# Performance work log

Measured on AMD Instinct MI355X. Metric: run time of the kernel, lower is better.

Reference implementation:

```python
import jax, jax.numpy as jnp
import numpy as np

B, N, M, K = 4, 8192, 2048, 8
F1, F2 = 256, 256


def _knn_idx(p1t, p2t, k):
    # p1t [B,N,3], p2t [B,M,3] -> idx [B,N,k] of k nearest points in p2t for each p1t point
    d = (jnp.sum(p1t ** 2, -1)[:, :, None]
         + jnp.sum(p2t ** 2, -1)[:, None, :]
         - 2.0 * jnp.einsum('bnc,bmc->bnm', p1t, p2t))
    _, idx = jax.lax.top_k(-d, k)
    return idx


def _gather(feat, idx):
    # feat [B,C,M], idx [B,N,K] -> [B,C,N,K]  (grouping_operation)
    return jax.vmap(lambda f, i: f[:, i])(feat, idx)


def setup_inputs() -> dict:
    key = jax.random.key(0)
    ks = jax.random.split(key, 16)
    rn = lambda k, s: jax.random.normal(k, s, dtype=jnp.float32)
    ru = lambda k, s: jax.random.uniform(k, s, dtype=jnp.float32)
    return {
        'pos1': rn(ks[0], (B, 3, N)),
        'pos2': rn(ks[1], (B, 3, M)),
        'feature1': rn(ks[2], (B, F1, N)),
        'feature2': rn(ks[3], (B, F2, M)),
        'w1_0': rn(ks[4], (128, F2 + 3)) * 0.05, 's1_0': ru(ks[5], (128,)), 'b1_0': rn(ks[6], (128,)) * 0.05,
        'w1_1': rn(ks[7], (128, 128)) * 0.05, 's1_1': ru(ks[8], (128,)), 'b1_1': rn(ks[9], (128,)) * 0.05,
        'w1_2': rn(ks[10], (256, 128)) * 0.05, 's1_2': ru(ks[11], (256,)), 'b1_2': rn(ks[12], (256,)) * 0.05,
        'w2_0': rn(ks[13], (256, 256 + F1)) * 0.05, 's2_0': ru(ks[14], (256,)), 'b2_0': rn(ks[15], (256,)) * 0.05,
    }


def reference(pos1, pos2, feature1, feature2,
              w1_0, s1_0, b1_0, w1_1, s1_1, b1_1, w1_2, s1_2, b1_2,
              w2_0, s2_0, b2_0):
    # KNN grouping (knn=True branch): neighbors of each pos1 point among pos2 points
    idx = _knn_idx(pos1.transpose(0, 2, 1), pos2.transpose(0, 2, 1), K)  # [B,N,K]
    pos2_grouped = _gather(pos2, idx)                 # [B,3,N,K]
    pos_diff = pos2_grouped - pos1[:, :, :, None]     # [B,3,N,K]
    feat2_grouped = _gather(feature2, idx)            # [B,F2,N,K]
    feat = jnp.concatenate([feat2_grouped, pos_diff], axis=1)  # [B,F2+3,N,K]
    # mlp1: 1x1 Conv2d (no bias) + BN(eval, folded scale/bias) + ReLU
    for w, s, b in ((w1_0, s1_0, b1_0), (w1_1, s1_1, b1_1), (w1_2, s1_2, b1_2)):
        feat = jax.nn.relu(jnp.einsum('oc,bcnk->bonk', w, feat)
                           * s[None, :, None, None] + b[None, :, None, None])
    feat = jnp.max(feat, axis=-1)                     # [B,256,N]
    feat = jnp.concatenate([feat, feature1], axis=1)  # [B,256+F1,N]
    # mlp2: 1x1 Conv1d (no bias) + BN + ReLU
    for w, s, b in ((w2_0, s2_0, b2_0),):
        feat = jax.nn.relu(jnp.einsum('oc,bcn->bon', w, feat)
                           * s[None, :, None] + b[None, :, None])
    return feat
```

## Files before the change

### kernel.cpp

```cpp
#include <hip/hip_runtime.h>
#include <hip/hip_bf16.h>

#define B_ 4
#define N_ 8192
#define M_ 2048
#define K_ 8

typedef __bf16 bf16x8 __attribute__((ext_vector_type(8)));
typedef __bf16 bf16x4 __attribute__((ext_vector_type(4)));
typedef float  floatx4 __attribute__((ext_vector_type(4)));

__global__ __launch_bounds__(256) void prep_weights(
    const float* __restrict__ w10, const float* __restrict__ w11,
    const float* __restrict__ w12, const float* __restrict__ w20,
    __bf16* __restrict__ w0p, __bf16* __restrict__ w11b,
    __bf16* __restrict__ w12b, __bf16* __restrict__ w20b)
{
  int t = blockIdx.x * 256 + threadIdx.x;
  if (t < 36864) {
    int o = t / 288, c = t - o * 288;
    w0p[t] = (c < 259) ? (__bf16)w10[o * 259 + c] : (__bf16)0.0f;
  } else if (t < 53248) {
    int i = t - 36864; w11b[i] = (__bf16)w11[i];
  } else if (t < 86016) {
    int i = t - 53248; w12b[i] = (__bf16)w12[i];
  } else if (t < 217088) {
    int i = t - 86016; w20b[i] = (__bf16)w20[i];
  }
}

__global__ __launch_bounds__(256) void transpose_cast(
    const float* __restrict__ in, __bf16* __restrict__ out, int C, int L)
{
  __shared__ float tile[32][33];
  const int b = blockIdx.z;
  const int c0 = blockIdx.y * 32, l0 = blockIdx.x * 32;
  const int tx = threadIdx.x & 31, ty = threadIdx.x >> 5;
  const float* src = in + (size_t)b * C * L;
  #pragma unroll
  for (int i = 0; i < 4; i++)
    tile[ty + 8 * i][tx] = src[(size_t)(c0 + ty + 8 * i) * L + l0 + tx];
  __syncthreads();
  __bf16* dst = out + (size_t)b * L * C;
  #pragma unroll
  for (int i = 0; i < 4; i++)
    dst[(size_t)(l0 + ty + 8 * i) * C + c0 + tx] = (__bf16)tile[tx][ty + 8 * i];
}

__global__ __launch_bounds__(256) void knn_kernel(
    const float* __restrict__ pos1, const float* __restrict__ pos2,
    int* __restrict__ idx_out)
{
  __shared__ floatx4 P[M_];
  __shared__ float md[64][33];
  __shared__ int   mi[64][33];
  const int b = blockIdx.y;
  const int n0 = blockIdx.x * 64;
  const int tid = threadIdx.x;

  const float* p2 = pos2 + b * 3 * M_;
  for (int i = tid; i < M_; i += 256) {
    float x = p2[i], y = p2[M_ + i], z = p2[2 * M_ + i];
    floatx4 q;
    q[0] = x; q[1] = y; q[2] = z;
    q[3] = __fadd_rn(__fadd_rn(__fmul_rn(x, x), __fmul_rn(y, y)), __fmul_rn(z, z));
    P[i] = q;
  }
  __syncthreads();

  const int p = tid >> 2, t = tid & 3;
  const int n = n0 + p;
  const float* p1 = pos1 + b * 3 * N_;
  const float x1 = p1[n], y1 = p1[N_ + n], z1 = p1[2 * N_ + n];
  const float r1 = __fadd_rn(__fadd_rn(__fmul_rn(x1, x1), __fmul_rn(y1, y1)),
                             __fmul_rn(z1, z1));

  float bd[K_]; int bi[K_];
  #pragma unroll
  for (int j = 0; j < K_; j++) { bd[j] = 3.0e38f; bi[j] = 0; }

  for (int j = 0; j < 512; j += 4) {
    float d4[4]; int c4[4];
    #pragma unroll
    for (int jj = 0; jj < 4; jj++) {
      const int c = t + 4 * (j + jj);
      floatx4 q = P[c];
      float dot = __fadd_rn(__fadd_rn(__fmul_rn(x1, q[0]), __fmul_rn(y1, q[1])),
                            __fmul_rn(z1, q[2]));
      d4[jj] = __fsub_rn(__fadd_rn(r1, q[3]), __fmul_rn(2.0f, dot));
      c4[jj] = c;
    }
    #pragma unroll
    for (int jj = 0; jj < 4; jj++) {
      float d = d4[jj];
      if (d < bd[K_ - 1]) {
        float cd = d; int ci = c4[jj];
        #pragma unroll
        for (int q = 0; q < K_; q++) {
          bool lt = (cd < bd[q]);
          float nd = lt ? cd : bd[q];  int ni = lt ? ci : bi[q];
          float od = lt ? bd[q] : cd;  int oi = lt ? bi[q] : ci;
          bd[q] = nd; bi[q] = ni; cd = od; ci = oi;
        }
      }
    }
  }
  #pragma unroll
  for (int r = 0; r < K_; r++) { md[p][t * 8 + r] = bd[r]; mi[p][t * 8 + r] = bi[r]; }
  __syncthreads();

  if (tid < 64) {
    int h[4] = {0, 0, 0, 0};
    int* o = idx_out + ((size_t)(b * N_ + n0 + tid)) * K_;
    for (int r = 0; r < K_; r++) {
      float bdv = 3.3e38f; int bii = 0x7fffffff; int bt = 0;
      #pragma unroll
      for (int tt = 0; tt < 4; tt++) {
        if (h[tt] < 8) {
          float dv = md[tid][tt * 8 + h[tt]];
          int   iv = mi[tid][tt * 8 + h[tt]];
          if (dv < bdv || (dv == bdv && iv < bii)) { bdv = dv; bii = iv; bt = tt; }
        }
      }
      #pragma unroll
      for (int tt = 0; tt < 4; tt++) h[tt] += (bt == tt);
      o[r] = bii;
    }
  }
}

template <int KSTEPS>
__device__ __forceinline__ void mfma_layer_lds(
    const __bf16* X, const __bf16* W, int wstride,
    const float* sv, const float* bv,
    __bf16* Y, int ycolbase, int c0, int lane)
{
  const int lrow = lane & 15, quad = lane >> 4;
  floatx4 acc[4][2];
  const floatx4 fz = {0.f, 0.f, 0.f, 0.f};
  #pragma unroll
  for (int pt = 0; pt < 4; pt++) { acc[pt][0] = fz; acc[pt][1] = fz; }

  bf16x8 wf0 = *(const bf16x8*)(W + (size_t)(c0 + lrow) * wstride + quad * 8);
  bf16x8 wf1 = *(const bf16x8*)(W + (size_t)(c0 + 16 + lrow) * wstride + quad * 8);
  bf16x8 xf[4];
  #pragma unroll
  for (int pt = 0; pt < 4; pt++)
    xf[pt] = *(const bf16x8*)(X + (pt * 16 + lrow) * 136 + quad * 8);

  #pragma unroll
  for (int ks = 0; ks < KSTEPS; ks++) {
    bf16x8 wn0, wn1, xn[4];
    if (ks + 1 < KSTEPS) {
      const int kn = (ks + 1) * 32 + quad * 8;
      wn0 = *(const bf16x8*)(W + (size_t)(c0 + lrow) * wstride + kn);
      wn1 = *(const bf16x8*)(W + (size_t)(c0 + 16 + lrow) * wstride + kn);
      #pragma unroll
      for (int pt = 0; pt < 4; pt++)
        xn[pt] = *(const bf16x8*)(X + (pt * 16 + lrow) * 136 + kn);
    }
    #pragma unroll
    for (int pt = 0; pt < 4; pt++) {
      acc[pt][0] = __builtin_amdgcn_mfma_f32_16x16x32_bf16(wf0, xf[pt], acc[pt][0], 0, 0, 0);
      acc[pt][1] = __builtin_amdgcn_mfma_f32_16x16x32_bf16(wf1, xf[pt], acc[pt][1], 0, 0, 0);
    }
    if (ks + 1 < KSTEPS) {
      wf0 = wn0; wf1 = wn1;
      #pragma unroll
      for (int pt = 0; pt < 4; pt++) xf[pt] = xn[pt];
    }
  }

  #pragma unroll
  for (int pt = 0; pt < 4; pt++) {
    #pragma unroll
    for (int wt = 0; wt < 2; wt++) {
      const int colg = c0 + wt * 16 + quad * 4;
      floatx4 s4 = *(const floatx4*)(sv + colg);
      floatx4 b4 = *(const floatx4*)(bv + colg);
      bf16x4 pk;
      #pragma unroll
      for (int r = 0; r < 4; r++) {
        float v = acc[pt][wt][r] * s4[r] + b4[r];
        pk[r] = (__bf16)(v > 0.f ? v : 0.f);
      }
      *(bf16x4*)(Y + (pt * 16 + lrow) * 136 + (colg - ycolbase)) = pk;
    }
  }
}

__global__ __launch_bounds__(256, 3) void mlp1_kernel(
    const float* __restrict__ pos1, const float* __restrict__ pos2,
    const int* __restrict__ idx, const __bf16* __restrict__ f2t,
    const __bf16* __restrict__ w0p, const float* __restrict__ s10, const float* __restrict__ b10,
    const __bf16* __restrict__ w11b, const float* __restrict__ s11, const float* __restrict__ b11,
    const __bf16* __restrict__ w12b, const float* __restrict__ s12, const float* __restrict__ b12,
    __bf16* __restrict__ maxed)
{
  __shared__ __align__(16) __bf16 Xs[64 * 256];
  __shared__ __align__(16) __bf16 Y0[64 * 136];
  __shared__ int mrow[64];
  __shared__ __align__(16) float dp[64][4];
  __bf16* const Y1 = Xs;

  const int b = blockIdx.y;
  const int n0 = blockIdx.x * 8;
  const int tid = threadIdx.x;
  const int wave = tid >> 6, lane = tid & 63;
  const int lrow = lane & 15, quad = lane >> 4;
  const int c0 = 32 * wave;

  if (tid < 64) {
    const int r = tid, g = r >> 3;
    const int m = idx[(b * N_ + n0) * K_ + r];
    mrow[r] = m;
    const int n = n0 + g;
    dp[r][0] = pos2[b * 3 * M_ + m]          - pos1[b * 3 * N_ + n];
    dp[r][1] = pos2[b * 3 * M_ + M_ + m]     - pos1[b * 3 * N_ + N_ + n];
    dp[r][2] = pos2[b * 3 * M_ + 2 * M_ + m] - pos1[b * 3 * N_ + 2 * N_ + n];
    dp[r][3] = 0.f;
  }
  __syncthreads();

  {
    const int r0 = wave * 16;
    const int half = lane >> 5;
    const int ch = lane & 31;
    #pragma unroll
    for (int i = 0; i < 8; i++) {
      const int r = r0 + 2 * i + half;
      const int m = mrow[r];
      const char* src = (const char*)f2t
          + (((size_t)(b * M_ + m)) << 9)
          + ((ch << 4) ^ ((r & 7) << 4));
      __builtin_amdgcn_global_load_lds(
          (const __attribute__((address_space(1))) unsigned int*)src,
          (__attribute__((address_space(3))) unsigned int*)(Xs + (r0 + 2 * i) * 256),
          16, 0, 0);
    }
  }

  bf16x8 xlast[4];
  #pragma unroll
  for (int pt = 0; pt < 4; pt++) {
    bf16x8 v = {};
    if (quad == 0) {
      floatx4 d = *(const floatx4*)(&dp[pt * 16 + lrow][0]);
      v[0] = (__bf16)d[0]; v[1] = (__bf16)d[1]; v[2] = (__bf16)d[2];
    }
    xlast[pt] = v;
  }

  bf16x8 wf0 = *(const bf16x8*)(w0p + (size_t)(c0 + lrow) * 288 + quad * 8);
  bf16x8 wf1 = *(const bf16x8*)(w0p + (size_t)(c0 + 16 + lrow) * 288 + quad * 8);

  __syncthreads();

  {
    floatx4 acc[4][2];
    const floatx4 fz = {0.f, 0.f, 0.f, 0.f};
    #pragma unroll
    for (int pt = 0; pt < 4; pt++) { acc[pt][0] = fz; acc[pt][1] = fz; }

    const int swz = (lrow & 7) << 4;
    bf16x8 xf[4];
    #pragma unroll
    for (int pt = 0; pt < 4; pt++)
      xf[pt] = *(const bf16x8*)((const char*)Xs + (pt * 16 + lrow) * 512
                                + ((quad * 16) ^ swz));

    #pragma unroll
    for (int ks = 0; ks < 9; ks++) {
      bf16x8 wn0, wn1, xn[4];
      if (ks < 8) {
        const int kn = (ks + 1) * 32 + quad * 8;
        wn0 = *(const bf16x8*)(w0p + (size_t)(c0 + lrow) * 288 + kn);
        wn1 = *(const bf16x8*)(w0p + (size_t)(c0 + 16 + lrow) * 288 + kn);
        if (ks < 7) {
          const int kb = ((ks + 1) * 64 + quad * 16) ^ swz;
          #pragma unroll
          for (int pt = 0; pt < 4; pt++)
            xn[pt] = *(const bf16x8*)((const char*)Xs + (pt * 16 + lrow) * 512 + kb);
        } else {
          #pragma unroll
          for (int pt = 0; pt < 4; pt++) xn[pt] = xlast[pt];
        }
      }
      #pragma unroll
      for (int pt = 0; pt < 4; pt++) {
        acc[pt][0] = __builtin_amdgcn_mfma_f32_16x16x32_bf16(wf0, xf[pt], acc[pt][0], 0, 0, 0);
        acc[pt][1] = __builtin_amdgcn_mfma_f32_16x16x32_bf16(wf1, xf[pt], acc[pt][1], 0, 0, 0);
      }
      if (ks < 8) {
        wf0 = wn0; wf1 = wn1;
        #pragma unroll
        for (int pt = 0; pt < 4; pt++) xf[pt] = xn[pt];
      }
    }
    #pragma unroll
    for (int pt = 0; pt < 4; pt++) {
      #pragma unroll
      for (int wt = 0; wt < 2; wt++) {
        const int colg = c0 + wt * 16 + quad * 4;
        floatx4 s4 = *(const floatx4*)(s10 + colg);
        floatx4 b4 = *(const floatx4*)(b10 + colg);
        bf16x4 pk;
        #pragma unroll
        for (int r = 0; r < 4; r++) {
          float v = acc[pt][wt][r] * s4[r] + b4[r];
          pk[r] = (__bf16)(v > 0.f ? v : 0.f);
        }
        *(bf16x4*)(Y0 + (pt * 16 + lrow) * 136 + colg) = pk;
      }
    }
  }
  __syncthreads();

  mfma_layer_lds<4>(Y0, w11b, 128, s11, b11, Y1, 0, c0, lane);
  __syncthreads();

  #pragma unroll
  for (int p = 0; p < 2; p++) {
    mfma_layer_lds<4>(Y1, w12b, 128, s12, b12, Y0, 128 * p, 128 * p + c0, lane);
    __syncthreads();
    if (tid < 128) {
      const int g = tid >> 4, cb = (tid & 15) * 8;
      bf16x8 v0 = *(const bf16x8*)(Y0 + (g * 8) * 136 + cb);
      float fmx[8];
      #pragma unroll
      for (int j = 0; j < 8; j++) fmx[j] = (float)v0[j];
      #pragma unroll
      for (int k = 1; k < 8; k++) {
        bf16x8 v = *(const bf16x8*)(Y0 + (g * 8 + k) * 136 + cb);
        #pragma unroll
        for (int j = 0; j < 8; j++) {
          float f = (float)v[j];
          fmx[j] = f > fmx[j] ? f : fmx[j];
        }
      }
      bf16x8 o;
      #pragma unroll
      for (int j = 0; j < 8; j++) o[j] = (__bf16)fmx[j];
      *(bf16x8*)(maxed + ((size_t)(b * N_ + n0 + g)) * 256 + 128 * p + cb) = o;
    }
    __syncthreads();
  }
}

__global__ __launch_bounds__(256, 6) void mlp2_kernel(
    const __bf16* __restrict__ maxed, const __bf16* __restrict__ f1t,
    const __bf16* __restrict__ w20b, const float* __restrict__ s20,
    const float* __restrict__ b20, float* __restrict__ out)
{
  const int rows0 = blockIdx.x * 32;
  const int b = rows0 >> 13;
  const int nbase = rows0 & (N_ - 1);
  const int tid = threadIdx.x;
  const int wave = tid >> 6, lane = tid & 63;
  const int lrow = lane & 15, quad = lane >> 4;
  const int c0 = 128 * blockIdx.y + 32 * wave;
  const floatx4 fz = {0.f, 0.f, 0.f, 0.f};

  floatx4 acc[2][2];
  acc[0][0] = fz; acc[0][1] = fz; acc[1][0] = fz; acc[1][1] = fz;

  auto aptr = [&](int ks, int mt) -> const __bf16* {
    const int k = ks * 32 + quad * 8;
    return (ks < 8) ? (maxed + (size_t)(rows0 + mt * 16 + lrow) * 256 + k)
                    : (f1t + (size_t)(rows0 + mt * 16 + lrow) * 256 + (k - 256));
  };

  bf16x8 w0 = *(const bf16x8*)(w20b + (size_t)(c0 + lrow) * 512 + quad * 8);
  bf16x8 w1 = *(const bf16x8*)(w20b + (size_t)(c0 + 16 + lrow) * 512 + quad * 8);
  bf16x8 a0 = *(const bf16x8*)aptr(0, 0);
  bf16x8 a1 = *(const bf16x8*)aptr(0, 1);

  #pragma unroll
  for (int ks = 0; ks < 16; ks++) {
    bf16x8 wn0, wn1, an0, an1;
    if (ks < 15) {
      const int kn = (ks + 1) * 32 + quad * 8;
      wn0 = *(const bf16x8*)(w20b + (size_t)(c0 + lrow) * 512 + kn);
      wn1 = *(const bf16x8*)(w20b + (size_t)(c0 + 16 + lrow) * 512 + kn);
      an0 = *(const bf16x8*)aptr(ks + 1, 0);
      an1 = *(const bf16x8*)aptr(ks + 1, 1);
    }
    acc[0][0] = __builtin_amdgcn_mfma_f32_16x16x32_bf16(a0, w0, acc[0][0], 0, 0, 0);
    acc[0][1] = __builtin_amdgcn_mfma_f32_16x16x32_bf16(a0, w1, acc[0][1], 0, 0, 0);
    acc[1][0] = __builtin_amdgcn_mfma_f32_16x16x32_bf16(a1, w0, acc[1][0], 0, 0, 0);
    acc[1][1] = __builtin_amdgcn_mfma_f32_16x16x32_bf16(a1, w1, acc[1][1], 0, 0, 0);
    if (ks < 15) { w0 = wn0; w1 = wn1; a0 = an0; a1 = an1; }
  }

  #pragma unroll
  for (int ct = 0; ct < 2; ct++) {
    const int col = c0 + ct * 16 + lrow;
    const float s = s20[col];
    const float bb = b20[col];
    #pragma unroll
    for (int mt = 0; mt < 2; mt++) {
      floatx4 pk;
      #pragma unroll
      for (int r = 0; r < 4; r++) {
        float v = acc[mt][ct][r] * s + bb;
        pk[r] = v > 0.f ? v : 0.f;
      }
      const int n = nbase + mt * 16 + quad * 4;
      *(floatx4*)(out + ((size_t)(b * 256 + col)) * N_ + n) = pk;
    }
  }
}

extern "C" void kernel_launch(void* const* d_in, const int* in_sizes, int n_in,
                              void* d_out, int out_size, void* d_ws, size_t ws_size,
                              hipStream_t stream)
{
  const float* pos1     = (const float*)d_in[0];
  const float* pos2     = (const float*)d_in[1];
  const float* feature1 = (const float*)d_in[2];
  const float* feature2 = (const float*)d_in[3];
  const float* w1_0 = (const float*)d_in[4];
  const float* s1_0 = (const float*)d_in[5];
  const float* b1_0 = (const float*)d_in[6];
  const float* w1_1 = (const float*)d_in[7];
  const float* s1_1 = (const float*)d_in[8];
  const float* b1_1 = (const float*)d_in[9];
  const float* w1_2 = (const float*)d_in[10];
  const float* s1_2 = (const float*)d_in[11];
  const float* b1_2 = (const float*)d_in[12];
  const float* w2_0 = (const float*)d_in[13];
  const float* s2_0 = (const float*)d_in[14];
  const float* b2_0 = (const float*)d_in[15];

  char* ws = (char*)d_ws;
  int*    idx   = (int*)(ws);
  __bf16* f2t   = (__bf16*)(ws + 1048576);
  __bf16* f1t   = (__bf16*)(ws + 5242880);
  __bf16* maxed = (__bf16*)(ws + 22020096);
  __bf16* w0p   = (__bf16*)(ws + 38797312);
  __bf16* w11b  = (__bf16*)(ws + 38871040);
  __bf16* w12b  = (__bf16*)(ws + 38903808);
  __bf16* w20b  = (__bf16*)(ws + 38969344);

  prep_weights<<<dim3(848), 256, 0, stream>>>(w1_0, w1_1, w1_2, w2_0,
                                              w0p, w11b, w12b, w20b);
  transpose_cast<<<dim3(M_ / 32, 8, B_), 256, 0, stream>>>(feature2, f2t, 256, M_);
  transpose_cast<<<dim3(N_ / 32, 8, B_), 256, 0, stream>>>(feature1, f1t, 256, N_);
  knn_kernel<<<dim3(N_ / 64, B_), 256, 0, stream>>>(pos1, pos2, idx);
  mlp1_kernel<<<dim3(N_ / 8, B_), 256, 0, stream>>>(
      pos1, pos2, idx, f2t, w0p, s1_0, b1_0, w11b, s1_1, b1_1, w12b, s1_2, b1_2, maxed);
  mlp2_kernel<<<dim3(1024, 2), 256, 0, stream>>>(maxed, f1t, w20b, s2_0, b2_0,
                                                 (float*)d_out);
}
```

Baseline: 369.9 us.

## Split KNN over two candidate halves with packed-key sorting networks and merge pass

The KNN kernel now handles half of the pos2 candidates per block (grid z=2), which doubles the block count and halves shared memory. Distance and index are packed into one 64-bit sortable key, and candidates are processed in batches of 8 with a sorting network plus a bitonic merge instead of per-candidate insertion. A new knn_merge kernel combines the two partial top-8 lists. This adds a kernel launch and a global round trip for the partial lists, which are stored in the 'maxed' workspace region before mlp1 overwrites it.

```diff
diff --git a/kernel.cpp b/kernel.cpp
--- a/kernel.cpp
+++ b/kernel.cpp
@@ -9,6 +9,7 @@
 typedef __bf16 bf16x8 __attribute__((ext_vector_type(8)));
 typedef __bf16 bf16x4 __attribute__((ext_vector_type(4)));
 typedef float  floatx4 __attribute__((ext_vector_type(4)));
+typedef unsigned long long u64k;
 
 __global__ __launch_bounds__(256) void prep_weights(
     const float* __restrict__ w10, const float* __restrict__ w11,
@@ -47,20 +48,28 @@
     dst[(size_t)(l0 + ty + 8 * i) * C + c0 + tx] = (__bf16)tile[tx][ty + 8 * i];
 }
 
-__global__ __launch_bounds__(256) void knn_kernel(
+__device__ __forceinline__ void ce(u64k& a, u64k& b) {
+  u64k lo = a < b ? a : b;
+  u64k hi = a < b ? b : a;
+  a = lo; b = hi;
+}
+
+__global__ __launch_bounds__(256, 4) void knn_kernel(
     const float* __restrict__ pos1, const float* __restrict__ pos2,
-    int* __restrict__ idx_out)
-{
-  __shared__ floatx4 P[M_];
-  __shared__ float md[64][33];
-  __shared__ int   mi[64][33];
+    u64k* __restrict__ part)
+{
+  __shared__ floatx4 P[1024];
+  __shared__ u64k md[64][33];
   const int b = blockIdx.y;
+  const int half = blockIdx.z;
   const int n0 = blockIdx.x * 64;
   const int tid = threadIdx.x;
+  const int cbase = half * 1024;
 
   const float* p2 = pos2 + b * 3 * M_;
-  for (int i = tid; i < M_; i += 256) {
-    float x = p2[i], y = p2[M_ + i], z = p2[2 * M_ + i];
+  for (int i = tid; i < 1024; i += 256) {
+    const int c = cbase + i;
+    float x = p2[c], y = p2[M_ + c], z = p2[2 * M_ + c];
     floatx4 q;
     q[0] = x; q[1] = y; q[2] = z;
     q[3] = __fadd_rn(__fadd_rn(__fmul_rn(x, x), __fmul_rn(y, y)), __fmul_rn(z, z));
@@ -75,58 +84,80 @@
   const float r1 = __fadd_rn(__fadd_rn(__fmul_rn(x1, x1), __fmul_rn(y1, y1)),
                              __fmul_rn(z1, z1));
 
-  float bd[K_]; int bi[K_];
-  #pragma unroll
-  for (int j = 0; j < K_; j++) { bd[j] = 3.0e38f; bi[j] = 0; }
-
-  for (int j = 0; j < 512; j += 4) {
-    float d4[4]; int c4[4];
-    #pragma unroll
-    for (int jj = 0; jj < 4; jj++) {
-      const int c = t + 4 * (j + jj);
-      floatx4 q = P[c];
-      float dot = __fadd_rn(__fadd_rn(__fmul_rn(x1, q[0]), __fmul_rn(y1, q[1])),
-                            __fmul_rn(z1, q[2]));
-      d4[jj] = __fsub_rn(__fadd_rn(r1, q[3]), __fmul_rn(2.0f, dot));
-      c4[jj] = c;
-    }
-    #pragma unroll
-    for (int jj = 0; jj < 4; jj++) {
-      float d = d4[jj];
-      if (d < bd[K_ - 1]) {
-        float cd = d; int ci = c4[jj];
-        #pragma unroll
-        for (int q = 0; q < K_; q++) {
-          bool lt = (cd < bd[q]);
-          float nd = lt ? cd : bd[q];  int ni = lt ? ci : bi[q];
-          float od = lt ? bd[q] : cd;  int oi = lt ? bi[q] : ci;
-          bd[q] = nd; bi[q] = ni; cd = od; ci = oi;
-        }
-      }
-    }
-  }
-  #pragma unroll
-  for (int r = 0; r < K_; r++) { md[p][t * 8 + r] = bd[r]; mi[p][t * 8 + r] = bi[r]; }
+  u64k bd[8];
+  #pragma unroll
+  for (int r = 0; r < 8; r++) bd[r] = ~0ULL;
+
+  for (int bb = 0; bb < 32; ++bb) {
+    floatx4 q[8];
+    #pragma unroll
+    for (int i = 0; i < 8; i++) q[i] = P[4 * (8 * bb + i) + t];
+
+    u64k s[8];
+    #pragma unroll
+    for (int i = 0; i < 8; i++) {
+      float dot = __fadd_rn(__fadd_rn(__fmul_rn(x1, q[i][0]), __fmul_rn(y1, q[i][1])),
+                            __fmul_rn(z1, q[i][2]));
+      float d = __fsub_rn(__fadd_rn(r1, q[i][3]), __fmul_rn(2.0f, dot));
+      unsigned du = __float_as_uint(d);
+      unsigned k32 = du ^ ((unsigned)((int)du >> 31) | 0x80000000u);
+      s[i] = ((u64k)k32 << 11) | (unsigned)(cbase + 4 * (8 * bb + i) + t);
+    }
+
+    ce(s[0], s[1]); ce(s[2], s[3]); ce(s[4], s[5]); ce(s[6], s[7]);
+    ce(s[0], s[2]); ce(s[1], s[3]); ce(s[4], s[6]); ce(s[5], s[7]);
+    ce(s[1], s[2]); ce(s[5], s[6]);
+    ce(s[0], s[4]); ce(s[1], s[5]); ce(s[2], s[6]); ce(s[3], s[7]);
+    ce(s[2], s[4]); ce(s[3], s[5]);
+    ce(s[1], s[2]); ce(s[3], s[4]); ce(s[5], s[6]);
+
+    if (s[0] < bd[7]) {
+      #pragma unroll
+      for (int k = 0; k < 8; k++) { u64k x = s[7 - k]; bd[k] = bd[k] < x ? bd[k] : x; }
+      ce(bd[0], bd[4]); ce(bd[1], bd[5]); ce(bd[2], bd[6]); ce(bd[3], bd[7]);
+      ce(bd[0], bd[2]); ce(bd[1], bd[3]); ce(bd[4], bd[6]); ce(bd[5], bd[7]);
+      ce(bd[0], bd[1]); ce(bd[2], bd[3]); ce(bd[4], bd[5]); ce(bd[6], bd[7]);
+    }
+  }
+
+  #pragma unroll
+  for (int r = 0; r < 8; r++) md[p][t * 8 + r] = bd[r];
   __syncthreads();
 
   if (tid < 64) {
-    int h[4] = {0, 0, 0, 0};
-    int* o = idx_out + ((size_t)(b * N_ + n0 + tid)) * K_;
-    for (int r = 0; r < K_; r++) {
-      float bdv = 3.3e38f; int bii = 0x7fffffff; int bt = 0;
-      #pragma unroll
-      for (int tt = 0; tt < 4; tt++) {
-        if (h[tt] < 8) {
-          float dv = md[tid][tt * 8 + h[tt]];
-          int   iv = mi[tid][tt * 8 + h[tt]];
-          if (dv < bdv || (dv == bdv && iv < bii)) { bdv = dv; bii = iv; bt = tt; }
-        }
-      }
-      #pragma unroll
-      for (int tt = 0; tt < 4; tt++) h[tt] += (bt == tt);
-      o[r] = bii;
-    }
-  }
+    int h0 = 0, h1 = 0, h2 = 0, h3 = 0;
+    u64k* o = part + ((size_t)((b * 2 + half) * N_ + n0 + tid)) * 8;
+    #pragma unroll
+    for (int r = 0; r < 8; r++) {
+      u64k k0 = md[tid][h0], k1 = md[tid][8 + h1];
+      u64k k2 = md[tid][16 + h2], k3 = md[tid][24 + h3];
+      u64k m01 = k0 < k1 ? k0 : k1;
+      u64k m23 = k2 < k3 ? k2 : k3;
+      u64k m = m01 < m23 ? m01 : m23;
+      h0 += (k0 == m); h1 += (k1 == m); h2 += (k2 == m); h3 += (k3 == m);
+      o[r] = m;
+    }
+  }
+}
+
+__global__ __launch_bounds__(256) void knn_merge(
+    const u64k* __restrict__ part, int* __restrict__ idx_out)
+{
+  const int pt = blockIdx.x * 256 + threadIdx.x;
+  const int b = pt >> 13, n = pt & (N_ - 1);
+  const u64k* a0 = part + ((size_t)((b * 2 + 0) * N_ + n)) * 8;
+  const u64k* a1 = part + ((size_t)((b * 2 + 1) * N_ + n)) * 8;
+  u64k av[8], cv[8];
+  #pragma unroll
+  for (int r = 0; r < 8; r++) { av[r] = a0[r]; cv[r] = a1[r]; }
+  #pragma unroll
+  for (int k = 0; k < 8; k++) { u64k x = cv[7 - k]; av[k] = av[k] < x ? av[k] : x; }
+  ce(av[0], av[4]); ce(av[1], av[5]); ce(av[2], av[6]); ce(av[3], av[7]);
+  ce(av[0], av[2]); ce(av[1], av[3]); ce(av[4], av[6]); ce(av[5], av[7]);
+  ce(av[0], av[1]); ce(av[2], av[3]); ce(av[4], av[5]); ce(av[6], av[7]);
+  int* o = idx_out + (size_t)pt * 8;
+  #pragma unroll
+  for (int r = 0; r < 8; r++) o[r] = (int)(av[r] & 2047u);
 }
 
 template <int KSTEPS>
@@ -441,12 +472,14 @@
   __bf16* w11b  = (__bf16*)(ws + 38871040);
   __bf16* w12b  = (__bf16*)(ws + 38903808);
   __bf16* w20b  = (__bf16*)(ws + 38969344);
+  u64k*   part  = (u64k*)(ws + 22020096);
 
   prep_weights<<<dim3(848), 256, 0, stream>>>(w1_0, w1_1, w1_2, w2_0,
                                               w0p, w11b, w12b, w20b);
   transpose_cast<<<dim3(M_ / 32, 8, B_), 256, 0, stream>>>(feature2, f2t, 256, M_);
   transpose_cast<<<dim3(N_ / 32, 8, B_), 256, 0, stream>>>(feature1, f1t, 256, N_);
-  knn_kernel<<<dim3(N_ / 64, B_), 256, 0, stream>>>(pos1, pos2, idx);
+  knn_kernel<<<dim3(N_ / 64, B_, 2), 256, 0, stream>>>(pos1, pos2, part);
+  knn_merge<<<dim3(N_ * B_ / 256), 256, 0, stream>>>(part, idx);
   mlp1_kernel<<<dim3(N_ / 8, B_), 256, 0, stream>>>(
       pos1, pos2, idx, f2t, w0p, s1_0, b1_0, w11b, s1_1, b1_1, w12b, s1_2, b1_2, maxed);
   mlp2_kernel<<<dim3(1024, 2), 256, 0, stream>>>(maxed, f1t, w20b, s2_0, b2_0,
```

Measured after the change: 340.0 us. 8.1% less time.
